# Kernel tuning notes

Hardware: AMD Instinct MI355X
Metric: run time of the kernel (lower is better)

Reference implementation:

```python
import jax, jax.numpy as jnp
import numpy as np

N_NODES = 50000
N_EDGES = 640000
N_SUPPORT = 3
D_IN = 128
D_OUT = 128


def setup_inputs() -> dict:
    key = jax.random.key(0)
    k = jax.random.split(key, 6)
    x = jax.random.normal(k[0], (N_NODES, D_IN), dtype=jnp.float32)
    edge_rows = jax.random.randint(k[1], (N_SUPPORT, N_EDGES), 0, N_NODES, dtype=jnp.int32)
    edge_cols = jax.random.randint(k[2], (N_SUPPORT, N_EDGES), 0, N_NODES, dtype=jnp.int32)
    edge_vals = jax.random.uniform(k[3], (N_SUPPORT, N_EDGES), dtype=jnp.float32)
    weights = jax.random.normal(k[4], (N_SUPPORT, D_IN, D_OUT), dtype=jnp.float32) * 0.05
    bias = jax.random.normal(k[5], (D_OUT,), dtype=jnp.float32) * 0.01
    return {"x": x, "edge_rows": edge_rows, "edge_cols": edge_cols,
            "edge_vals": edge_vals, "weights": weights, "bias": bias}


def reference(x, edge_rows, edge_cols, edge_vals, weights, bias):
    # Dense projection per support: [S, N, D_OUT]
    pre = jnp.einsum('nd,sdo->sno', x, weights)

    def spmm(rows, cols, vals, dense):
        # sparse [N,N] @ dense [N,D] via gather + scatter-add
        msgs = vals[:, None] * dense[cols]          # [E, D]
        return jax.ops.segment_sum(msgs, rows, num_segments=dense.shape[0])

    out = jax.vmap(spmm)(edge_rows, edge_cols, edge_vals, pre).sum(axis=0)
    return jax.nn.relu(out + bias)
```

## Files before the change

### kernel.cpp

```cpp
#include <hip/hip_runtime.h>

#define N_NODES 50000
#define N_EDGES 640000
#define N_SUP   3
#define D       128
#define NTOT    150000
#define E_TOT   1920000
#define NC      293
#define CAPC    7680
#define CTILE   2048
#define CTPS    313
#define SBLKS   (N_SUP * CTPS)
#define XCBLKS  3125
#define WBLKS   96
#define LDSTR   132

typedef __attribute__((ext_vector_type(2))) float f32x2;
typedef __attribute__((ext_vector_type(4))) float f32x4;
typedef __attribute__((ext_vector_type(8))) short s16x8;

__device__ __forceinline__ unsigned short f2bf(float f) {
    unsigned int u = __float_as_uint(f);
    u += 0x7FFFu + ((u >> 16) & 1u);
    return (unsigned short)(u >> 16);
}

__global__ __launch_bounds__(512) void prep_scatter(
    const int* __restrict__ rows, const int* __restrict__ cols,
    const float* __restrict__ vals, int* __restrict__ coarse_wptr,
    unsigned int* __restrict__ sortedM, unsigned short* __restrict__ sortedV,
    const float4* __restrict__ x, ushort4* __restrict__ xb,
    const float* __restrict__ W, unsigned short* __restrict__ Wf)
{
    int tid = threadIdx.x;

    if (blockIdx.x >= SBLKS) {
        int gid = (blockIdx.x - SBLKS) * 512 + tid;
        if (gid < N_NODES * D / 4) {
            float4 v = x[gid];
            ushort4 o;
            o.x = f2bf(v.x); o.y = f2bf(v.y); o.z = f2bf(v.z); o.w = f2bf(v.w);
            xb[gid] = o;
        } else {
            int g2 = gid - N_NODES * D / 4;
            if (g2 < N_SUP * D * D) {
                int j    = g2 & 7;
                int lane = (g2 >> 3) & 63;
                int rest = g2 >> 9;
                int nt = rest & 7, kb = (rest >> 3) & 3, s = rest >> 5;
                int k = kb * 32 + ((lane >> 4) * 8) + j;
                int n = nt * 16 + (lane & 15);
                Wf[g2] = f2bf(W[((size_t)s * D + k) * D + n]);
            }
        }
        return;
    }

    __shared__ int            h[512];
    __shared__ int            toff[512];
    __shared__ int            gbase[512];
    __shared__ int            wsum[8];
    __shared__ unsigned int   stageM[CTILE];
    __shared__ unsigned short stageV[CTILE];
    __shared__ unsigned int   dst[CTILE];

    const int lane = tid & 63;
    const int w    = tid >> 6;

    h[tid] = 0;
    __syncthreads();

    int s  = blockIdx.x / CTPS;
    int tb = (blockIdx.x % CTPS) * CTILE;
    int n  = N_EDGES - tb; if (n > CTILE) n = CTILE;
    const int*   rp = rows + (size_t)s * N_EDGES + tb;
    const int*   cp = cols + (size_t)s * N_EDGES + tb;
    const float* vp = vals + (size_t)s * N_EDGES + tb;

    int bk[4], rk[4]; unsigned int edM[4]; unsigned short edV[4];
    #pragma unroll
    for (int i = 0; i < 4; ++i) {
        int idx = tid + i * 512;
        bk[i] = -1;
        if (idx < n) {
            int grow = s * N_NODES + rp[idx];
            bk[i] = grow >> 9;
            rk[i] = atomicAdd(&h[bk[i]], 1);
            edM[i] = ((unsigned int)(grow & 511) << 16) | (unsigned int)cp[idx];
            edV[i] = f2bf(vp[idx]);
        }
    }
    __syncthreads();
    int cntb = h[tid];

    int v = cntb;
    #pragma unroll
    for (int d = 1; d < 64; d <<= 1) {
        int t = __shfl_up(v, d);
        v += (lane >= d) ? t : 0;
    }
    if (lane == 63) wsum[w] = v;
    __syncthreads();
    int add = 0;
    #pragma unroll
    for (int i = 0; i < 8; ++i) add += (i < w) ? wsum[i] : 0;
    int incl = v + add;

    toff[tid]  = incl - cntb;
    gbase[tid] = (cntb > 0) ? atomicAdd(&coarse_wptr[tid * 16], cntb) : 0;
    __syncthreads();

    #pragma unroll
    for (int i = 0; i < 4; ++i) {
        if (bk[i] >= 0) {
            int slot  = toff[bk[i]] + rk[i];
            int gslot = gbase[bk[i]] + rk[i];
            stageM[slot] = edM[i];
            stageV[slot] = edV[i];
            dst[slot] = (gslot < CAPC)
                      ? (unsigned int)(bk[i] * CAPC + gslot)
                      : 0xFFFFFFFFu;
        }
    }
    __syncthreads();
    for (int j = tid; j < n; j += 512) {
        unsigned int d = dst[j];
        if (d != 0xFFFFFFFFu) {
            sortedM[d] = stageM[j];
            sortedV[d] = stageV[j];
        }
    }
}

__global__ __launch_bounds__(512) void bucket_sort(
    const int* __restrict__ coarse_wptr,
    const unsigned int* __restrict__ sortedM,
    const unsigned short* __restrict__ sortedV,
    int* __restrict__ row_ptr2, unsigned int* __restrict__ sortedB)
{
    int c   = blockIdx.x;
    int cnt = coarse_wptr[c * 16];
    if (cnt > CAPC) cnt = CAPC;

    __shared__ int hist[512];
    __shared__ int rank[512];
    __shared__ int wsum[8];
    int tid  = threadIdx.x;
    int lane = tid & 63;
    int w    = tid >> 6;
    hist[tid] = 0;

    const unsigned int*   srcM = sortedM + (size_t)c * CAPC;
    const unsigned short* srcV = sortedV + (size_t)c * CAPC;
    unsigned int   m[15];
    unsigned short vv[15];
    #pragma unroll
    for (int k = 0; k < 15; ++k) {
        int idx = tid + k * 512;
        if (idx < cnt) { m[k] = srcM[idx]; vv[k] = srcV[idx]; }
    }
    __syncthreads();
    #pragma unroll
    for (int k = 0; k < 15; ++k) {
        int idx = tid + k * 512;
        if (idx < cnt) atomicAdd(&hist[m[k] >> 16], 1);
    }
    __syncthreads();

    int cntb = hist[tid];
    int v = cntb;
    #pragma unroll
    for (int d = 1; d < 64; d <<= 1) {
        int t = __shfl_up(v, d);
        v += (lane >= d) ? t : 0;
    }
    if (lane == 63) wsum[w] = v;
    __syncthreads();
    int add = 0;
    #pragma unroll
    for (int i = 0; i < 8; ++i) add += (i < w) ? wsum[i] : 0;
    int incl = v + add;

    int start = c * CAPC + incl - cntb;
    rank[tid] = start;
    row_ptr2[c * 513 + tid] = start;
    if (tid == 511) row_ptr2[c * 513 + 512] = c * CAPC + incl;
    __syncthreads();

    #pragma unroll
    for (int k = 0; k < 15; ++k) {
        int idx = tid + k * 512;
        if (idx < cnt) {
            int r = atomicAdd(&rank[m[k] >> 16], 1);
            sortedB[r] = ((unsigned int)vv[k] << 16) | (m[k] & 0xFFFFu);
        }
    }
}

__global__ __launch_bounds__(256) void gather_gemm(
    const unsigned short* __restrict__ xb, const int* __restrict__ row_ptr2,
    const unsigned int* __restrict__ sortedB,
    const unsigned short* __restrict__ Wf,
    const float* __restrict__ bias, float* __restrict__ out)
{
    __shared__ unsigned short ys[48 * LDSTR];
    __shared__ int rs[48], re[48];
    const int tid  = threadIdx.x;
    const int w    = tid >> 6;
    const int lane = tid & 63;
    const int m0   = blockIdx.x * 16;

    if (tid < 48) {
        int grow = (tid >> 4) * N_NODES + m0 + (tid & 15);
        int rpi  = (grow >> 9) * 513 + (grow & 511);
        rs[tid] = row_ptr2[rpi];
        re[tid] = row_ptr2[rpi + 1];
    }
    __syncthreads();

    const int hh = lane >> 5;
    const int u  = lane & 31;
    for (int r = w; r < 48; r += 4) {
        int start = rs[r], end = re[r];
        f32x2 accA = {0.f, 0.f}, accB = {0.f, 0.f};
        for (int j = start; j < end; j += 64) {
            int m = end - j; if (m > 64) m = 64;
            unsigned int ev = (lane < m) ? sortedB[j + lane] : 0u;
            for (int t = 0; t < m; t += 4) {
                unsigned int e0 = (unsigned int)__shfl((int)ev, t + hh);
                unsigned int e1 = (unsigned int)__shfl((int)ev, t + 2 + hh);
                float v0 = __uint_as_float(e0 & 0xFFFF0000u);
                float v1 = __uint_as_float(e1 & 0xFFFF0000u);
                uint2 X0 = *((const uint2*)(xb + (size_t)(e0 & 0xFFFFu) * D) + u);
                uint2 X1 = *((const uint2*)(xb + (size_t)(e1 & 0xFFFFu) * D) + u);
                f32x2 xa0 = {__uint_as_float(X0.x << 16),
                             __uint_as_float(X0.x & 0xFFFF0000u)};
                f32x2 xb0 = {__uint_as_float(X0.y << 16),
                             __uint_as_float(X0.y & 0xFFFF0000u)};
                f32x2 xa1 = {__uint_as_float(X1.x << 16),
                             __uint_as_float(X1.x & 0xFFFF0000u)};
                f32x2 xb1 = {__uint_as_float(X1.y << 16),
                             __uint_as_float(X1.y & 0xFFFF0000u)};
                accA += v0 * xa0;
                accB += v0 * xb0;
                accA += v1 * xa1;
                accB += v1 * xb1;
            }
        }
        float a0 = accA.x, a1 = accA.y, a2 = accB.x, a3 = accB.y;
        a0 += __shfl_xor(a0, 32);
        a1 += __shfl_xor(a1, 32);
        a2 += __shfl_xor(a2, 32);
        a3 += __shfl_xor(a3, 32);
        if (hh == 0) {
            uint2 o;
            o.x = (unsigned int)f2bf(a0) | ((unsigned int)f2bf(a1) << 16);
            o.y = (unsigned int)f2bf(a2) | ((unsigned int)f2bf(a3) << 16);
            *(uint2*)(ys + r * LDSTR + u * 4) = o;
        }
    }
    __syncthreads();

    const int quad = lane >> 4;
    const int l16  = lane & 15;
    const int nt0  = w * 2;
    f32x4 acc0 = {0.f, 0.f, 0.f, 0.f}, acc1 = {0.f, 0.f, 0.f, 0.f};

    #pragma unroll
    for (int s = 0; s < N_SUP; ++s) {
        #pragma unroll
        for (int kb = 0; kb < 4; ++kb) {
            union { uint2 q[2]; s16x8 v; } A;
            const unsigned short* ap = ys + (s * 16 + l16) * LDSTR
                                          + kb * 32 + quad * 8;
            A.q[0] = *(const uint2*)ap;
            A.q[1] = *(const uint2*)(ap + 4);
            const unsigned short* wf = Wf + (size_t)((s * 4 + kb) * 8 + nt0) * 64 * 8
                                          + lane * 8;
            s16x8 b0 = *(const s16x8*)wf;
            s16x8 b1 = *(const s16x8*)(wf + 64 * 8);
            acc0 = __builtin_amdgcn_mfma_f32_16x16x32_bf16(A.v, b0, acc0, 0, 0, 0);
            acc1 = __builtin_amdgcn_mfma_f32_16x16x32_bf16(A.v, b1, acc1, 0, 0, 0);
        }
    }

    #pragma unroll
    for (int p = 0; p < 2; ++p) {
        int col = (nt0 + p) * 16 + l16;
        float bv = bias[col];
        f32x4 a = p ? acc1 : acc0;
        #pragma unroll
        for (int r = 0; r < 4; ++r) {
            int row = m0 + quad * 4 + r;
            out[(size_t)row * D + col] = fmaxf(a[r] + bv, 0.f);
        }
    }
}

extern "C" void kernel_launch(void* const* d_in, const int* in_sizes, int n_in,
                              void* d_out, int out_size, void* d_ws, size_t ws_size,
                              hipStream_t stream)
{
    const float* x         = (const float*)d_in[0];
    const int*   edge_rows = (const int*)  d_in[1];
    const int*   edge_cols = (const int*)  d_in[2];
    const float* edge_vals = (const float*)d_in[3];
    const float* weights   = (const float*)d_in[4];
    const float* bias      = (const float*)d_in[5];
    float* out = (float*)d_out;

    char* ws = (char*)d_ws;
    size_t off = 0;
    auto alloc = [&](size_t bytes) -> char* {
        char* p = ws + off;
        off += (bytes + 255) & ~(size_t)255;
        return p;
    };
    int*            coarse_wptr = (int*)            alloc(512 * 16 * 4);
    int*            row_ptr2    = (int*)            alloc((size_t)NC * 513 * 4);
    unsigned short* xb          = (unsigned short*) alloc((size_t)N_NODES * D * 2);
    unsigned short* Wf          = (unsigned short*) alloc((size_t)N_SUP * D * D * 2);
    unsigned int*   sortedM     = (unsigned int*)   alloc((size_t)NC * CAPC * 4);
    unsigned short* sortedV     = (unsigned short*) alloc((size_t)NC * CAPC * 2);
    unsigned int*   sortedB     = (unsigned int*)   alloc((size_t)NC * CAPC * 4);

    hipMemsetAsync(coarse_wptr, 0, 512 * 16 * 4, stream);
    prep_scatter<<<SBLKS + XCBLKS + WBLKS, 512, 0, stream>>>(
        edge_rows, edge_cols, edge_vals, coarse_wptr, sortedM, sortedV,
        (const float4*)x, (ushort4*)xb, weights, Wf);
    bucket_sort <<<NC, 512, 0, stream>>>(coarse_wptr, sortedM, sortedV,
                                         row_ptr2, sortedB);
    gather_gemm<<<N_NODES / 16, 256, 0, stream>>>(xb, row_ptr2, sortedB,
                                                  Wf, bias, out);
}
```

Baseline: 199.1 us.

## Replace atomic bucket allocation with per-tile histogram and cross-tile scan

Splits the edge scatter into three kernels. The first builds per-tile bucket histograms, fused with the bf16 conversion of x and W. The second scans each bucket's counts across tiles. The third scatters edges to their precomputed global offsets, which removes the global atomicAdd on coarse_wptr and its memset and makes the bucket layout deterministic. In exchange, edge rows are read twice, the tile histogram makes an extra round trip through global memory, and there are more kernel launches. Separately, bucket_sort now uses 1024 threads per block, with 8 elements per thread instead of 15, to lower register pressure and add parallelism.

```diff
diff --git a/kernel.cpp b/kernel.cpp
--- a/kernel.cpp
+++ b/kernel.cpp
@@ -11,6 +11,7 @@
 #define CTILE   2048
 #define CTPS    313
 #define SBLKS   (N_SUP * CTPS)
+#define HP      320
 #define XCBLKS  3125
 #define WBLKS   96
 #define LDSTR   132
@@ -25,10 +26,8 @@
     return (unsigned short)(u >> 16);
 }
 
-__global__ __launch_bounds__(512) void prep_scatter(
-    const int* __restrict__ rows, const int* __restrict__ cols,
-    const float* __restrict__ vals, int* __restrict__ coarse_wptr,
-    unsigned int* __restrict__ sortedM, unsigned short* __restrict__ sortedV,
+__global__ __launch_bounds__(512) void hist_convert(
+    const int* __restrict__ rows, int* __restrict__ tileHist,
     const float4* __restrict__ x, ushort4* __restrict__ xb,
     const float* __restrict__ W, unsigned short* __restrict__ Wf)
 {
@@ -56,6 +55,62 @@
         return;
     }
 
+    __shared__ int h[512];
+    h[tid] = 0;
+    __syncthreads();
+
+    int s  = blockIdx.x / CTPS;
+    int tb = (blockIdx.x % CTPS) * CTILE;
+    int n  = N_EDGES - tb; if (n > CTILE) n = CTILE;
+    const int* rp = rows + (size_t)s * N_EDGES + tb;
+
+    #pragma unroll
+    for (int i = 0; i < 4; ++i) {
+        int idx = tid + i * 512;
+        if (idx < n) atomicAdd(&h[(s * N_NODES + rp[idx]) >> 9], 1);
+    }
+    __syncthreads();
+    if (tid < NC) tileHist[(size_t)blockIdx.x * HP + tid] = h[tid];
+}
+
+__global__ __launch_bounds__(512) void scan_tiles(
+    int* __restrict__ tileHist, int* __restrict__ bucketCnt)
+{
+    __shared__ int wsum[8];
+    int b    = blockIdx.x;
+    int tid  = threadIdx.x;
+    int lane = tid & 63;
+    int w    = tid >> 6;
+    int t0   = 2 * tid, t1 = 2 * tid + 1;
+
+    int a = (t0 < SBLKS) ? tileHist[(size_t)t0 * HP + b] : 0;
+    int c = (t1 < SBLKS) ? tileHist[(size_t)t1 * HP + b] : 0;
+    int s = a + c;
+
+    int v = s;
+    #pragma unroll
+    for (int d = 1; d < 64; d <<= 1) {
+        int t = __shfl_up(v, d);
+        v += (lane >= d) ? t : 0;
+    }
+    if (lane == 63) wsum[w] = v;
+    __syncthreads();
+    int add = 0;
+    #pragma unroll
+    for (int i = 0; i < 8; ++i) add += (i < w) ? wsum[i] : 0;
+    int incl = v + add;
+    int excl = incl - s;
+
+    if (t0 < SBLKS) tileHist[(size_t)t0 * HP + b] = excl;
+    if (t1 < SBLKS) tileHist[(size_t)t1 * HP + b] = excl + a;
+    if (tid == 511) bucketCnt[b] = incl;
+}
+
+__global__ __launch_bounds__(512) void scatter(
+    const int* __restrict__ rows, const int* __restrict__ cols,
+    const float* __restrict__ vals, const int* __restrict__ tileHist,
+    unsigned int* __restrict__ sortedM, unsigned short* __restrict__ sortedV)
+{
     __shared__ int            h[512];
     __shared__ int            toff[512];
     __shared__ int            gbase[512];
@@ -64,10 +119,12 @@
     __shared__ unsigned short stageV[CTILE];
     __shared__ unsigned int   dst[CTILE];
 
+    int tid  = threadIdx.x;
     const int lane = tid & 63;
     const int w    = tid >> 6;
 
     h[tid] = 0;
+    if (tid < NC) gbase[tid] = tileHist[(size_t)blockIdx.x * HP + tid];
     __syncthreads();
 
     int s  = blockIdx.x / CTPS;
@@ -104,10 +161,7 @@
     int add = 0;
     #pragma unroll
     for (int i = 0; i < 8; ++i) add += (i < w) ? wsum[i] : 0;
-    int incl = v + add;
-
-    toff[tid]  = incl - cntb;
-    gbase[tid] = (cntb > 0) ? atomicAdd(&coarse_wptr[tid * 16], cntb) : 0;
+    toff[tid] = v + add - cntb;
     __syncthreads();
 
     #pragma unroll
@@ -132,14 +186,14 @@
     }
 }
 
-__global__ __launch_bounds__(512) void bucket_sort(
-    const int* __restrict__ coarse_wptr,
+__global__ __launch_bounds__(1024) void bucket_sort(
+    const int* __restrict__ bucketCnt,
     const unsigned int* __restrict__ sortedM,
     const unsigned short* __restrict__ sortedV,
     int* __restrict__ row_ptr2, unsigned int* __restrict__ sortedB)
 {
     int c   = blockIdx.x;
-    int cnt = coarse_wptr[c * 16];
+    int cnt = bucketCnt[c];
     if (cnt > CAPC) cnt = CAPC;
 
     __shared__ int hist[512];
@@ -148,48 +202,52 @@
     int tid  = threadIdx.x;
     int lane = tid & 63;
     int w    = tid >> 6;
-    hist[tid] = 0;
+    if (tid < 512) hist[tid] = 0;
 
     const unsigned int*   srcM = sortedM + (size_t)c * CAPC;
     const unsigned short* srcV = sortedV + (size_t)c * CAPC;
-    unsigned int   m[15];
-    unsigned short vv[15];
-    #pragma unroll
-    for (int k = 0; k < 15; ++k) {
-        int idx = tid + k * 512;
+    unsigned int   m[8];
+    unsigned short vv[8];
+    #pragma unroll
+    for (int k = 0; k < 8; ++k) {
+        int idx = tid + k * 1024;
         if (idx < cnt) { m[k] = srcM[idx]; vv[k] = srcV[idx]; }
     }
     __syncthreads();
     #pragma unroll
-    for (int k = 0; k < 15; ++k) {
-        int idx = tid + k * 512;
+    for (int k = 0; k < 8; ++k) {
+        int idx = tid + k * 1024;
         if (idx < cnt) atomicAdd(&hist[m[k] >> 16], 1);
     }
     __syncthreads();
 
-    int cntb = hist[tid];
-    int v = cntb;
-    #pragma unroll
-    for (int d = 1; d < 64; d <<= 1) {
-        int t = __shfl_up(v, d);
-        v += (lane >= d) ? t : 0;
-    }
-    if (lane == 63) wsum[w] = v;
-    __syncthreads();
-    int add = 0;
-    #pragma unroll
-    for (int i = 0; i < 8; ++i) add += (i < w) ? wsum[i] : 0;
-    int incl = v + add;
-
-    int start = c * CAPC + incl - cntb;
-    rank[tid] = start;
-    row_ptr2[c * 513 + tid] = start;
-    if (tid == 511) row_ptr2[c * 513 + 512] = c * CAPC + incl;
-    __syncthreads();
-
-    #pragma unroll
-    for (int k = 0; k < 15; ++k) {
-        int idx = tid + k * 512;
+    int cntb = 0, v = 0;
+    if (tid < 512) {
+        cntb = hist[tid];
+        v = cntb;
+        #pragma unroll
+        for (int d = 1; d < 64; d <<= 1) {
+            int t = __shfl_up(v, d);
+            v += (lane >= d) ? t : 0;
+        }
+        if (lane == 63) wsum[w] = v;
+    }
+    __syncthreads();
+    if (tid < 512) {
+        int add = 0;
+        #pragma unroll
+        for (int i = 0; i < 8; ++i) add += (i < w) ? wsum[i] : 0;
+        int incl  = v + add;
+        int start = c * CAPC + incl - cntb;
+        rank[tid] = start;
+        row_ptr2[c * 513 + tid] = start;
+        if (tid == 511) row_ptr2[c * 513 + 512] = c * CAPC + incl;
+    }
+    __syncthreads();
+
+    #pragma unroll
+    for (int k = 0; k < 8; ++k) {
+        int idx = tid + k * 1024;
         if (idx < cnt) {
             int r = atomicAdd(&rank[m[k] >> 16], 1);
             sortedB[r] = ((unsigned int)vv[k] << 16) | (m[k] & 0xFFFFu);
@@ -316,20 +374,22 @@
         off += (bytes + 255) & ~(size_t)255;
         return p;
     };
-    int*            coarse_wptr = (int*)            alloc(512 * 16 * 4);
-    int*            row_ptr2    = (int*)            alloc((size_t)NC * 513 * 4);
-    unsigned short* xb          = (unsigned short*) alloc((size_t)N_NODES * D * 2);
-    unsigned short* Wf          = (unsigned short*) alloc((size_t)N_SUP * D * D * 2);
-    unsigned int*   sortedM     = (unsigned int*)   alloc((size_t)NC * CAPC * 4);
-    unsigned short* sortedV     = (unsigned short*) alloc((size_t)NC * CAPC * 2);
-    unsigned int*   sortedB     = (unsigned int*)   alloc((size_t)NC * CAPC * 4);
-
-    hipMemsetAsync(coarse_wptr, 0, 512 * 16 * 4, stream);
-    prep_scatter<<<SBLKS + XCBLKS + WBLKS, 512, 0, stream>>>(
-        edge_rows, edge_cols, edge_vals, coarse_wptr, sortedM, sortedV,
-        (const float4*)x, (ushort4*)xb, weights, Wf);
-    bucket_sort <<<NC, 512, 0, stream>>>(coarse_wptr, sortedM, sortedV,
-                                         row_ptr2, sortedB);
-    gather_gemm<<<N_NODES / 16, 256, 0, stream>>>(xb, row_ptr2, sortedB,
-                                                  Wf, bias, out);
-}
+    int*            tileHist  = (int*)            alloc((size_t)SBLKS * HP * 4);
+    int*            bucketCnt = (int*)            alloc((size_t)NC * 4);
+    int*            row_ptr2  = (int*)            alloc((size_t)NC * 513 * 4);
+    unsigned short* xb        = (unsigned short*) alloc((size_t)N_NODES * D * 2);
+    unsigned short* Wf        = (unsigned short*) alloc((size_t)N_SUP * D * D * 2);
+    unsigned int*   sortedM   = (unsigned int*)   alloc((size_t)NC * CAPC * 4);
+    unsigned short* sortedV   = (unsigned short*) alloc((size_t)NC * CAPC * 2);
+    unsigned int*   sortedB   = (unsigned int*)   alloc((size_t)NC * CAPC * 4);
+
+    hist_convert<<<SBLKS + XCBLKS + WBLKS, 512, 0, stream>>>(
+        edge_rows, tileHist, (const float4*)x, (ushort4*)xb, weights, Wf);
+    scan_tiles  <<<NC, 512, 0, stream>>>(tileHist, bucketCnt);
+    scatter     <<<SBLKS, 512, 0, stream>>>(edge_rows, edge_cols, edge_vals,
+                                            tileHist, sortedM, sortedV);
+    bucket_sort <<<NC, 1024, 0, stream>>>(bucketCnt, sortedM, sortedV,
+                                          row_ptr2, sortedB);
+    gather_gemm <<<N_NODES / 16, 256, 0, stream>>>(xb, row_ptr2, sortedB,
+                                                   Wf, bias, out);
+}
```

New measurement: 201.8 us. Within noise of the previous version (+1.3%).

## Move x/W bf16 conversion into bucket sort kernel and pack edges as uint2

Applied to the files above, without the earlier changes.

The x and W float-to-bf16 conversion blocks move out of the scatter kernel and into the second-stage bucket-sort kernel, so the light sort work (293 blocks) shares a launch with the bandwidth-bound conversion. The intermediate edge record becomes a single uint2 (meta plus value) instead of separate 4-byte and 2-byte arrays, giving one wider store and load per edge. In exchange the intermediate buffer grows from 6 to 8 bytes per slot, adding write and read traffic, and the scatter kernel now runs on its own.

```diff
diff --git a/kernel.cpp b/kernel.cpp
--- a/kernel.cpp
+++ b/kernel.cpp
@@ -28,14 +28,91 @@
 __global__ __launch_bounds__(512) void prep_scatter(
     const int* __restrict__ rows, const int* __restrict__ cols,
     const float* __restrict__ vals, int* __restrict__ coarse_wptr,
-    unsigned int* __restrict__ sortedM, unsigned short* __restrict__ sortedV,
+    uint2* __restrict__ sortedA)
+{
+    __shared__ int          h[512];
+    __shared__ int          toff[512];
+    __shared__ int          gbase[512];
+    __shared__ int          wsum[8];
+    __shared__ uint2        stage[CTILE];
+    __shared__ unsigned int dst[CTILE];
+
+    int tid  = threadIdx.x;
+    const int lane = tid & 63;
+    const int w    = tid >> 6;
+
+    h[tid] = 0;
+    __syncthreads();
+
+    int s  = blockIdx.x / CTPS;
+    int tb = (blockIdx.x % CTPS) * CTILE;
+    int n  = N_EDGES - tb; if (n > CTILE) n = CTILE;
+    const int*   rp = rows + (size_t)s * N_EDGES + tb;
+    const int*   cp = cols + (size_t)s * N_EDGES + tb;
+    const float* vp = vals + (size_t)s * N_EDGES + tb;
+
+    int bk[4], rk[4]; uint2 ed[4];
+    #pragma unroll
+    for (int i = 0; i < 4; ++i) {
+        int idx = tid + i * 512;
+        bk[i] = -1;
+        if (idx < n) {
+            int grow = s * N_NODES + rp[idx];
+            bk[i] = grow >> 9;
+            rk[i] = atomicAdd(&h[bk[i]], 1);
+            ed[i] = make_uint2(((unsigned int)(grow & 511) << 16)
+                               | (unsigned int)cp[idx],
+                               (unsigned int)f2bf(vp[idx]) << 16);
+        }
+    }
+    __syncthreads();
+    int cntb = h[tid];
+
+    int v = cntb;
+    #pragma unroll
+    for (int d = 1; d < 64; d <<= 1) {
+        int t = __shfl_up(v, d);
+        v += (lane >= d) ? t : 0;
+    }
+    if (lane == 63) wsum[w] = v;
+    __syncthreads();
+    int add = 0;
+    #pragma unroll
+    for (int i = 0; i < 8; ++i) add += (i < w) ? wsum[i] : 0;
+    int incl = v + add;
+
+    toff[tid]  = incl - cntb;
+    gbase[tid] = (cntb > 0) ? atomicAdd(&coarse_wptr[tid * 16], cntb) : 0;
+    __syncthreads();
+
+    #pragma unroll
+    for (int i = 0; i < 4; ++i) {
+        if (bk[i] >= 0) {
+            int slot  = toff[bk[i]] + rk[i];
+            int gslot = gbase[bk[i]] + rk[i];
+            stage[slot] = ed[i];
+            dst[slot] = (gslot < CAPC)
+                      ? (unsigned int)(bk[i] * CAPC + gslot)
+                      : 0xFFFFFFFFu;
+        }
+    }
+    __syncthreads();
+    for (int j = tid; j < n; j += 512) {
+        unsigned int d = dst[j];
+        if (d != 0xFFFFFFFFu) sortedA[d] = stage[j];
+    }
+}
+
+__global__ __launch_bounds__(512) void sort_convert(
+    const int* __restrict__ coarse_wptr, const uint2* __restrict__ sortedA,
+    int* __restrict__ row_ptr2, unsigned int* __restrict__ sortedB,
     const float4* __restrict__ x, ushort4* __restrict__ xb,
     const float* __restrict__ W, unsigned short* __restrict__ Wf)
 {
     int tid = threadIdx.x;
 
-    if (blockIdx.x >= SBLKS) {
-        int gid = (blockIdx.x - SBLKS) * 512 + tid;
+    if (blockIdx.x >= NC) {
+        int gid = (blockIdx.x - NC) * 512 + tid;
         if (gid < N_NODES * D / 4) {
             float4 v = x[gid];
             ushort4 o;
@@ -56,88 +133,6 @@
         return;
     }
 
-    __shared__ int            h[512];
-    __shared__ int            toff[512];
-    __shared__ int            gbase[512];
-    __shared__ int            wsum[8];
-    __shared__ unsigned int   stageM[CTILE];
-    __shared__ unsigned short stageV[CTILE];
-    __shared__ unsigned int   dst[CTILE];
-
-    const int lane = tid & 63;
-    const int w    = tid >> 6;
-
-    h[tid] = 0;
-    __syncthreads();
-
-    int s  = blockIdx.x / CTPS;
-    int tb = (blockIdx.x % CTPS) * CTILE;
-    int n  = N_EDGES - tb; if (n > CTILE) n = CTILE;
-    const int*   rp = rows + (size_t)s * N_EDGES + tb;
-    const int*   cp = cols + (size_t)s * N_EDGES + tb;
-    const float* vp = vals + (size_t)s * N_EDGES + tb;
-
-    int bk[4], rk[4]; unsigned int edM[4]; unsigned short edV[4];
-    #pragma unroll
-    for (int i = 0; i < 4; ++i) {
-        int idx = tid + i * 512;
-        bk[i] = -1;
-        if (idx < n) {
-            int grow = s * N_NODES + rp[idx];
-            bk[i] = grow >> 9;
-            rk[i] = atomicAdd(&h[bk[i]], 1);
-            edM[i] = ((unsigned int)(grow & 511) << 16) | (unsigned int)cp[idx];
-            edV[i] = f2bf(vp[idx]);
-        }
-    }
-    __syncthreads();
-    int cntb = h[tid];
-
-    int v = cntb;
-    #pragma unroll
-    for (int d = 1; d < 64; d <<= 1) {
-        int t = __shfl_up(v, d);
-        v += (lane >= d) ? t : 0;
-    }
-    if (lane == 63) wsum[w] = v;
-    __syncthreads();
-    int add = 0;
-    #pragma unroll
-    for (int i = 0; i < 8; ++i) add += (i < w) ? wsum[i] : 0;
-    int incl = v + add;
-
-    toff[tid]  = incl - cntb;
-    gbase[tid] = (cntb > 0) ? atomicAdd(&coarse_wptr[tid * 16], cntb) : 0;
-    __syncthreads();
-
-    #pragma unroll
-    for (int i = 0; i < 4; ++i) {
-        if (bk[i] >= 0) {
-            int slot  = toff[bk[i]] + rk[i];
-            int gslot = gbase[bk[i]] + rk[i];
-            stageM[slot] = edM[i];
-            stageV[slot] = edV[i];
-            dst[slot] = (gslot < CAPC)
-                      ? (unsigned int)(bk[i] * CAPC + gslot)
-                      : 0xFFFFFFFFu;
-        }
-    }
-    __syncthreads();
-    for (int j = tid; j < n; j += 512) {
-        unsigned int d = dst[j];
-        if (d != 0xFFFFFFFFu) {
-            sortedM[d] = stageM[j];
-            sortedV[d] = stageV[j];
-        }
-    }
-}
-
-__global__ __launch_bounds__(512) void bucket_sort(
-    const int* __restrict__ coarse_wptr,
-    const unsigned int* __restrict__ sortedM,
-    const unsigned short* __restrict__ sortedV,
-    int* __restrict__ row_ptr2, unsigned int* __restrict__ sortedB)
-{
     int c   = blockIdx.x;
     int cnt = coarse_wptr[c * 16];
     if (cnt > CAPC) cnt = CAPC;
@@ -145,25 +140,22 @@
     __shared__ int hist[512];
     __shared__ int rank[512];
     __shared__ int wsum[8];
-    int tid  = threadIdx.x;
     int lane = tid & 63;
     int w    = tid >> 6;
     hist[tid] = 0;
 
-    const unsigned int*   srcM = sortedM + (size_t)c * CAPC;
-    const unsigned short* srcV = sortedV + (size_t)c * CAPC;
-    unsigned int   m[15];
-    unsigned short vv[15];
+    const uint2* src = sortedA + (size_t)c * CAPC;
+    uint2 e[15];
     #pragma unroll
     for (int k = 0; k < 15; ++k) {
         int idx = tid + k * 512;
-        if (idx < cnt) { m[k] = srcM[idx]; vv[k] = srcV[idx]; }
+        if (idx < cnt) e[k] = src[idx];
     }
     __syncthreads();
     #pragma unroll
     for (int k = 0; k < 15; ++k) {
         int idx = tid + k * 512;
-        if (idx < cnt) atomicAdd(&hist[m[k] >> 16], 1);
+        if (idx < cnt) atomicAdd(&hist[e[k].x >> 16], 1);
     }
     __syncthreads();
 
@@ -191,8 +183,8 @@
     for (int k = 0; k < 15; ++k) {
         int idx = tid + k * 512;
         if (idx < cnt) {
-            int r = atomicAdd(&rank[m[k] >> 16], 1);
-            sortedB[r] = ((unsigned int)vv[k] << 16) | (m[k] & 0xFFFFu);
+            int r = atomicAdd(&rank[e[k].x >> 16], 1);
+            sortedB[r] = (e[k].y & 0xFFFF0000u) | (e[k].x & 0xFFFFu);
         }
     }
 }
@@ -320,16 +312,15 @@
     int*            row_ptr2    = (int*)            alloc((size_t)NC * 513 * 4);
     unsigned short* xb          = (unsigned short*) alloc((size_t)N_NODES * D * 2);
     unsigned short* Wf          = (unsigned short*) alloc((size_t)N_SUP * D * D * 2);
-    unsigned int*   sortedM     = (unsigned int*)   alloc((size_t)NC * CAPC * 4);
-    unsigned short* sortedV     = (unsigned short*) alloc((size_t)NC * CAPC * 2);
+    uint2*          sortedA     = (uint2*)          alloc((size_t)NC * CAPC * 8);
     unsigned int*   sortedB     = (unsigned int*)   alloc((size_t)NC * CAPC * 4);
 
     hipMemsetAsync(coarse_wptr, 0, 512 * 16 * 4, stream);
-    prep_scatter<<<SBLKS + XCBLKS + WBLKS, 512, 0, stream>>>(
-        edge_rows, edge_cols, edge_vals, coarse_wptr, sortedM, sortedV,
+    prep_scatter<<<SBLKS, 512, 0, stream>>>(
+        edge_rows, edge_cols, edge_vals, coarse_wptr, sortedA);
+    sort_convert<<<NC + XCBLKS + WBLKS, 512, 0, stream>>>(
+        coarse_wptr, sortedA, row_ptr2, sortedB,
         (const float4*)x, (ushort4*)xb, weights, Wf);
-    bucket_sort <<<NC, 512, 0, stream>>>(coarse_wptr, sortedM, sortedV,
-                                         row_ptr2, sortedB);
     gather_gemm<<<N_NODES / 16, 256, 0, stream>>>(xb, row_ptr2, sortedB,
                                                   Wf, bias, out);
 }
```

Measured after the change: 195.5 us. Within noise of the previous version (-1.8%).
